# Kernel tuning notes

Measured on AMD Instinct MI355X. Metric: run time of the kernel, lower is better.

The kernel has to match this reference:

```python
import jax, jax.numpy as jnp
import numpy as np

NUM_NODES = 200000
EMB_DIM = 64
NUM_EDGES = 6400000
NUM_LAYERS = 4


def setup_inputs() -> dict:
    key = jax.random.key(0)
    k1, k2, k3, k4 = jax.random.split(key, 4)
    embeds = jax.random.normal(k1, (NUM_NODES, EMB_DIM), dtype=jnp.float32)
    adj_rows = jax.random.randint(k2, (NUM_EDGES,), 0, NUM_NODES, dtype=jnp.int64)
    adj_cols = jax.random.randint(k3, (NUM_EDGES,), 0, NUM_NODES, dtype=jnp.int64)
    adj_vals = jax.random.uniform(k4, (NUM_EDGES,), dtype=jnp.float32)
    return {"embeds": embeds, "adj_rows": adj_rows, "adj_cols": adj_cols, "adj_vals": adj_vals}


def _spmm(rows, cols, vals, x):
    # Sparse (COO) adjacency @ dense x: out[r] += v * x[c]
    msgs = vals[:, None] * x[cols]  # [E, d] gather + scale
    return jax.ops.segment_sum(msgs, rows, num_segments=NUM_NODES)


def reference(embeds, adj_rows, adj_cols, adj_vals):
    x = embeds
    acc = x  # running sum over layer outputs (fuses stack+mean)
    for _ in range(NUM_LAYERS):
        x = _spmm(adj_rows, adj_cols, adj_vals, x)
        acc = acc + x
    return acc / jnp.float32(NUM_LAYERS + 1)
```

## Files before the change

kernel.cpp:

```cpp
#include <hip/hip_runtime.h>

#define N_NODES 200000
#define DIM 64
#define BSHIFT 8
#define BROWS 256
#define NB 782
#define NB_PAD 1024
#define CHUNK 4096

__device__ __forceinline__ float bf2f(unsigned short u) {
    return __uint_as_float(((unsigned int)u) << 16);
}
__device__ __forceinline__ unsigned short f2bf(float f) {
    unsigned int u = __float_as_uint(f);
    u += 0x7FFFu + ((u >> 16) & 1u);
    return (unsigned short)(u >> 16);
}

__global__ __launch_bounds__(256) void bucket_hist(const int* __restrict__ rows, int E,
                                                   int* __restrict__ bcnt) {
    __shared__ int h[NB_PAD];
    for (int i = threadIdx.x; i < NB_PAD; i += 256) h[i] = 0;
    __syncthreads();
    int stride = gridDim.x * blockDim.x;
    for (int e = blockIdx.x * blockDim.x + threadIdx.x; e < E; e += stride)
        atomicAdd(&h[rows[e] >> BSHIFT], 1);
    __syncthreads();
    for (int i = threadIdx.x; i < NB; i += 256)
        if (h[i]) atomicAdd(&bcnt[i], h[i]);
}

__global__ __launch_bounds__(1024) void bucket_scan(const int* __restrict__ bcnt,
                                                    int* __restrict__ bbase,
                                                    int* __restrict__ bcur) {
    __shared__ int wsum[16];
    int t = threadIdx.x;
    int v = (t < NB) ? bcnt[t] : 0;
    int incl = v;
    for (int off = 1; off < 64; off <<= 1) {
        int u = __shfl_up(incl, off);
        if ((t & 63) >= off) incl += u;
    }
    if ((t & 63) == 63) wsum[t >> 6] = incl;
    __syncthreads();
    if (t < 16) {
        int w = wsum[t];
        for (int off = 1; off < 16; off <<= 1) {
            int u = __shfl_up(w, off);
            if (t >= off) w += u;
        }
        wsum[t] = w;
    }
    __syncthreads();
    int wb = (t >= 64) ? wsum[(t >> 6) - 1] : 0;
    int excl = wb + incl - v;
    if (t < NB) { bbase[t] = excl; bcur[t] = excl; }
    if (t == NB - 1) bbase[NB] = excl + v;
}

__global__ __launch_bounds__(512) void bucket_scatter(const int* __restrict__ rows,
                                                      const int* __restrict__ cols,
                                                      const float* __restrict__ vals, int E,
                                                      int* __restrict__ bcur,
                                                      int2* __restrict__ tmp) {
    __shared__ int h[NB_PAD];
    __shared__ int cur2[NB_PAD];
    __shared__ int wtot[8];
    __shared__ int2 stage[CHUNK];
    __shared__ unsigned short sbkt[CHUNK];
    const int base = blockIdx.x * CHUNK;
    const int count = min(CHUNK, E - base);
    const int t = threadIdx.x;

    for (int i = t; i < NB_PAD; i += 512) h[i] = 0;
    __syncthreads();

    int myr[8], myc[8];
    float myv[8];
#pragma unroll
    for (int k = 0; k < 8; ++k) {
        int i = t + k * 512;
        if (i < count) {
            myr[k] = rows[base + i];
            myc[k] = cols[base + i];
            myv[k] = vals[base + i];
            atomicAdd(&h[myr[k] >> BSHIFT], 1);
        }
    }
    __syncthreads();

    int h0 = h[2 * t], h1 = h[2 * t + 1];
    int s = h0 + h1;
    int incl = s;
    for (int off = 1; off < 64; off <<= 1) {
        int u = __shfl_up(incl, off);
        if ((t & 63) >= off) incl += u;
    }
    if ((t & 63) == 63) wtot[t >> 6] = incl;
    __syncthreads();
    int wb = 0;
    for (int w = 0; w < (t >> 6); ++w) wb += wtot[w];
    int excl = wb + incl - s;
    cur2[2 * t] = excl;
    cur2[2 * t + 1] = excl + h0;
    __syncthreads();

    for (int i = t; i < NB; i += 512) {
        int hi = h[i];
        int g = hi ? atomicAdd(&bcur[i], hi) : 0;
        h[i] = g - cur2[i];
    }
    __syncthreads();

#pragma unroll
    for (int k = 0; k < 8; ++k) {
        int i = t + k * 512;
        if (i < count) {
            int r = myr[k];
            int b = r >> BSHIFT;
            int slot = atomicAdd(&cur2[b], 1);
            stage[slot] = make_int2(((r & (BROWS - 1)) << 18) | myc[k], __float_as_int(myv[k]));
            sbkt[slot] = (unsigned short)b;
        }
    }
    __syncthreads();
    for (int s2 = t; s2 < count; s2 += 512)
        tmp[s2 + h[sbkt[s2]]] = stage[s2];
}

__global__ __launch_bounds__(512) void bucket_sort(const int2* __restrict__ tmp,
                                                   const int* __restrict__ bbase,
                                                   int2* __restrict__ sorted,
                                                   int* __restrict__ row_start) {
    __shared__ int h[BROWS];
    __shared__ int hbase[BROWS];
    __shared__ int wtot[4];
    const int b = blockIdx.x;
    const int s0 = bbase[b], s1 = bbase[b + 1];
    const int t = threadIdx.x;
    if (t < BROWS) h[t] = 0;
    __syncthreads();
    for (int e = s0 + t; e < s1; e += 512)
        atomicAdd(&h[tmp[e].x >> 18], 1);
    __syncthreads();
    int v = 0, incl = 0;
    if (t < BROWS) {
        v = h[t];
        incl = v;
        for (int off = 1; off < 64; off <<= 1) {
            int u = __shfl_up(incl, off);
            if ((t & 63) >= off) incl += u;
        }
        if ((t & 63) == 63) wtot[t >> 6] = incl;
    }
    __syncthreads();
    if (t < BROWS) {
        int wb = 0;
        for (int w = 0; w < (t >> 6); ++w) wb += wtot[w];
        hbase[t] = wb + incl - v;
    }
    __syncthreads();
    if (t < BROWS) {
        h[t] = hbase[t];
        int row = (b << BSHIFT) + t;
        if (row < N_NODES) row_start[row] = s0 + hbase[t];
    }
    if (b == NB - 1 && t == 0) row_start[N_NODES] = s1;
    __syncthreads();
    for (int e = s0 + t; e < s1; e += 512) {
        int2 kv = tmp[e];
        int r = kv.x >> 18;
        int rank = atomicAdd(&h[r], 1);
        sorted[s0 + rank] = make_int2(kv.x & 0x3FFFF, kv.y);
    }
}

__global__ __launch_bounds__(256) void convert_kernel(const float* __restrict__ src,
                                                      unsigned short* __restrict__ dst, int n4) {
    int i = blockIdx.x * blockDim.x + threadIdx.x;
    if (i >= n4) return;
    float4 v = *(const float4*)(src + i * 4);
    ushort4 o;
    o.x = f2bf(v.x); o.y = f2bf(v.y); o.z = f2bf(v.z); o.w = f2bf(v.w);
    *(ushort4*)(dst + i * 4) = o;
}

#define BF_LO(u) __uint_as_float((u) << 16)
#define BF_HI(u) __uint_as_float((u) & 0xFFFF0000u)
#define FMA8(G, V)                              \
    do {                                        \
        a0 = fmaf((V), BF_LO((G).x), a0);       \
        a1 = fmaf((V), BF_HI((G).x), a1);       \
        a2 = fmaf((V), BF_LO((G).y), a2);       \
        a3 = fmaf((V), BF_HI((G).y), a3);       \
        a4 = fmaf((V), BF_LO((G).z), a4);       \
        a5 = fmaf((V), BF_HI((G).z), a5);       \
        a6 = fmaf((V), BF_LO((G).w), a6);       \
        a7 = fmaf((V), BF_HI((G).w), a7);       \
    } while (0)

template <int MODE>
__global__ __launch_bounds__(256) void spmm_kernel(const int2* __restrict__ sorted,
                                                   const int* __restrict__ row_start,
                                                   const unsigned short* __restrict__ xb,
                                                   const float* __restrict__ embeds,
                                                   unsigned short* __restrict__ y,
                                                   float* __restrict__ acc) {
    int gid = blockIdx.x * blockDim.x + threadIdx.x;
    int r = gid >> 3;
    if (r >= N_NODES) return;
    int j = (gid & 7) << 3;
    const unsigned short* xbj = xb + j;
    int e = row_start[r], eend = row_start[r + 1];
    float a0 = 0.f, a1 = 0.f, a2 = 0.f, a3 = 0.f, a4 = 0.f, a5 = 0.f, a6 = 0.f, a7 = 0.f;

    int2 c0 = make_int2(0, 0), c1 = make_int2(0, 0);
    int2 c2 = make_int2(0, 0), c3 = make_int2(0, 0);
    if (e + 4 <= eend) {
        c0 = sorted[e]; c1 = sorted[e + 1]; c2 = sorted[e + 2]; c3 = sorted[e + 3];
    }
    while (e + 8 <= eend) {
        uint4 g0 = *(const uint4*)(xbj + (c0.x << 6));
        uint4 g1 = *(const uint4*)(xbj + (c1.x << 6));
        uint4 g2 = *(const uint4*)(xbj + (c2.x << 6));
        uint4 g3 = *(const uint4*)(xbj + (c3.x << 6));
        int2 n0 = sorted[e + 4], n1 = sorted[e + 5];
        int2 n2 = sorted[e + 6], n3 = sorted[e + 7];
        float v0 = __int_as_float(c0.y), v1 = __int_as_float(c1.y);
        float v2 = __int_as_float(c2.y), v3 = __int_as_float(c3.y);
        FMA8(g0, v0); FMA8(g1, v1); FMA8(g2, v2); FMA8(g3, v3);
        c0 = n0; c1 = n1; c2 = n2; c3 = n3;
        e += 4;
    }
    if (e + 4 <= eend) {
        uint4 g0 = *(const uint4*)(xbj + (c0.x << 6));
        uint4 g1 = *(const uint4*)(xbj + (c1.x << 6));
        uint4 g2 = *(const uint4*)(xbj + (c2.x << 6));
        uint4 g3 = *(const uint4*)(xbj + (c3.x << 6));
        float v0 = __int_as_float(c0.y), v1 = __int_as_float(c1.y);
        float v2 = __int_as_float(c2.y), v3 = __int_as_float(c3.y);
        FMA8(g0, v0); FMA8(g1, v1); FMA8(g2, v2); FMA8(g3, v3);
        e += 4;
    }
    for (; e < eend; ++e) {
        int2 cv = sorted[e];
        uint4 g = *(const uint4*)(xbj + (cv.x << 6));
        float v = __int_as_float(cv.y);
        FMA8(g, v);
    }

    int o = (r << 6) + j;
    if (MODE == 0) {
        uint4 yo;
        yo.x = (unsigned)f2bf(a0) | ((unsigned)f2bf(a1) << 16);
        yo.y = (unsigned)f2bf(a2) | ((unsigned)f2bf(a3) << 16);
        yo.z = (unsigned)f2bf(a4) | ((unsigned)f2bf(a5) << 16);
        yo.w = (unsigned)f2bf(a6) | ((unsigned)f2bf(a7) << 16);
        *(uint4*)(y + o) = yo;
        float4 x0 = *(const float4*)(embeds + o);
        float4 x1 = *(const float4*)(embeds + o + 4);
        *(float4*)(acc + o)     = make_float4(x0.x + a0, x0.y + a1, x0.z + a2, x0.w + a3);
        *(float4*)(acc + o + 4) = make_float4(x1.x + a4, x1.y + a5, x1.z + a6, x1.w + a7);
    } else if (MODE == 1) {
        uint4 yo;
        yo.x = (unsigned)f2bf(a0) | ((unsigned)f2bf(a1) << 16);
        yo.y = (unsigned)f2bf(a2) | ((unsigned)f2bf(a3) << 16);
        yo.z = (unsigned)f2bf(a4) | ((unsigned)f2bf(a5) << 16);
        yo.w = (unsigned)f2bf(a6) | ((unsigned)f2bf(a7) << 16);
        *(uint4*)(y + o) = yo;
        float4 q0 = *(const float4*)(acc + o);
        float4 q1 = *(const float4*)(acc + o + 4);
        *(float4*)(acc + o)     = make_float4(q0.x + a0, q0.y + a1, q0.z + a2, q0.w + a3);
        *(float4*)(acc + o + 4) = make_float4(q1.x + a4, q1.y + a5, q1.z + a6, q1.w + a7);
    } else {
        const float sc = 0.2f;
        float4 q0 = *(const float4*)(acc + o);
        float4 q1 = *(const float4*)(acc + o + 4);
        *(float4*)(acc + o)     = make_float4((q0.x + a0) * sc, (q0.y + a1) * sc,
                                              (q0.z + a2) * sc, (q0.w + a3) * sc);
        *(float4*)(acc + o + 4) = make_float4((q1.x + a4) * sc, (q1.y + a5) * sc,
                                              (q1.z + a6) * sc, (q1.w + a7) * sc);
    }
}

extern "C" void kernel_launch(void* const* d_in, const int* in_sizes, int n_in,
                              void* d_out, int out_size, void* d_ws, size_t ws_size,
                              hipStream_t stream) {
    const float* embeds = (const float*)d_in[0];
    const int*   rows   = (const int*)d_in[1];
    const int*   cols   = (const int*)d_in[2];
    const float* vals   = (const float*)d_in[3];
    float* acc = (float*)d_out;
    const int E = in_sizes[1];

    char* ws = (char*)d_ws;
    size_t off = 0;
    auto alloc = [&](size_t bytes) -> char* {
        char* p = ws + off;
        off = (off + bytes + 255) & ~(size_t)255;
        return p;
    };
    int*   bcnt      = (int*)alloc((size_t)NB * 4);
    int*   bbase     = (int*)alloc((size_t)(NB + 1) * 4);
    int*   bcur      = (int*)alloc((size_t)NB * 4);
    int*   row_start = (int*)alloc((size_t)(N_NODES + 1) * 4);
    int2*  sorted    = (int2*)alloc((size_t)E * 8);
    unsigned short* xb0 = (unsigned short*)alloc((size_t)N_NODES * DIM * 2);
    unsigned short* xb1 = (unsigned short*)alloc((size_t)N_NODES * DIM * 2);
    int2*  tmp       = (int2*)alloc((size_t)E * 8);

    hipMemsetAsync(bcnt, 0, (size_t)NB * 4, stream);

    bucket_hist<<<1024, 256, 0, stream>>>(rows, E, bcnt);
    bucket_scan<<<1, 1024, 0, stream>>>(bcnt, bbase, bcur);
    bucket_scatter<<<(E + CHUNK - 1) / CHUNK, 512, 0, stream>>>(rows, cols, vals, E, bcur, tmp);
    bucket_sort<<<NB, 512, 0, stream>>>(tmp, bbase, sorted, row_start);

    int n4 = N_NODES * DIM / 4;
    convert_kernel<<<(n4 + 255) / 256, 256, 0, stream>>>(embeds, xb0, n4);

    int sb = (N_NODES * 8 + 255) / 256;
    spmm_kernel<0><<<sb, 256, 0, stream>>>(sorted, row_start, xb0, embeds, xb1, acc);
    spmm_kernel<1><<<sb, 256, 0, stream>>>(sorted, row_start, xb1, embeds, xb0, acc);
    spmm_kernel<1><<<sb, 256, 0, stream>>>(sorted, row_start, xb0, embeds, xb1, acc);
    spmm_kernel<2><<<sb, 256, 0, stream>>>(sorted, row_start, xb1, embeds, xb0, acc);
}
```

Measured before the change: 823.2 us.

## Partition edges into column stripes for per-row CSR segments per stripe

Edges are now bucketed by column stripe (8 stripes of 25000 nodes) and then by destination-row block, producing eight CSR row_start arrays, one per stripe. In SpMM each row walks stripe 0 through 7 in turn, so threads running at similar times gather from the same 25000-node slice of x and that slice can stay resident in cache. The costs are a bigger sort (3128 buckets, more bucket_sort blocks, a smaller scatter chunk), eight row_start reads per row, and the loss of the old software prefetch of the next edge group. Because stripes are processed in order within each row, rows run concurrently are not kept on the same stripe, so the gain in cache locality is uncertain.

Result: slower. 895.3 us (+8.8%).

```diff
diff --git a/kernel.cpp b/kernel.cpp
--- a/kernel.cpp
+++ b/kernel.cpp
@@ -2,31 +2,36 @@
 
 #define N_NODES 200000
 #define DIM 64
-#define BSHIFT 8
-#define BROWS 256
-#define NB 782
-#define NB_PAD 1024
-#define CHUNK 4096
-
-__device__ __forceinline__ float bf2f(unsigned short u) {
-    return __uint_as_float(((unsigned int)u) << 16);
-}
+#define NS 8
+#define SROWS 25000
+#define DSHIFT 9
+#define DROWS 512
+#define NDB 391
+#define NB2 (NS * NDB)
+#define NB2_PAD 4096
+#define CHUNK 2048
+#define RSP (N_NODES + 1)
+
 __device__ __forceinline__ unsigned short f2bf(float f) {
     unsigned int u = __float_as_uint(f);
     u += 0x7FFFu + ((u >> 16) & 1u);
     return (unsigned short)(u >> 16);
 }
-
-__global__ __launch_bounds__(256) void bucket_hist(const int* __restrict__ rows, int E,
+__device__ __forceinline__ int stripe_of(int c) { return (int)((unsigned)c / 25000u); }
+
+__global__ __launch_bounds__(256) void bucket_hist(const int* __restrict__ rows,
+                                                   const int* __restrict__ cols, int E,
                                                    int* __restrict__ bcnt) {
-    __shared__ int h[NB_PAD];
-    for (int i = threadIdx.x; i < NB_PAD; i += 256) h[i] = 0;
+    __shared__ int h[NB2];
+    for (int i = threadIdx.x; i < NB2; i += 256) h[i] = 0;
     __syncthreads();
     int stride = gridDim.x * blockDim.x;
-    for (int e = blockIdx.x * blockDim.x + threadIdx.x; e < E; e += stride)
-        atomicAdd(&h[rows[e] >> BSHIFT], 1);
-    __syncthreads();
-    for (int i = threadIdx.x; i < NB; i += 256)
+    for (int e = blockIdx.x * blockDim.x + threadIdx.x; e < E; e += stride) {
+        int cb = stripe_of(cols[e]) * NDB + (rows[e] >> DSHIFT);
+        atomicAdd(&h[cb], 1);
+    }
+    __syncthreads();
+    for (int i = threadIdx.x; i < NB2; i += 256)
         if (h[i]) atomicAdd(&bcnt[i], h[i]);
 }
 
@@ -35,8 +40,13 @@
                                                     int* __restrict__ bcur) {
     __shared__ int wsum[16];
     int t = threadIdx.x;
-    int v = (t < NB) ? bcnt[t] : 0;
-    int incl = v;
+    int idx = 4 * t;
+    int v0 = (idx + 0 < NB2) ? bcnt[idx + 0] : 0;
+    int v1 = (idx + 1 < NB2) ? bcnt[idx + 1] : 0;
+    int v2 = (idx + 2 < NB2) ? bcnt[idx + 2] : 0;
+    int v3 = (idx + 3 < NB2) ? bcnt[idx + 3] : 0;
+    int ssum = v0 + v1 + v2 + v3;
+    int incl = ssum;
     for (int off = 1; off < 64; off <<= 1) {
         int u = __shfl_up(incl, off);
         if ((t & 63) >= off) incl += u;
@@ -53,9 +63,14 @@
     }
     __syncthreads();
     int wb = (t >= 64) ? wsum[(t >> 6) - 1] : 0;
-    int excl = wb + incl - v;
-    if (t < NB) { bbase[t] = excl; bcur[t] = excl; }
-    if (t == NB - 1) bbase[NB] = excl + v;
+    int run = wb + incl - ssum;
+    if (idx + 0 < NB2) { bbase[idx + 0] = run; bcur[idx + 0] = run; } else if (idx + 0 == NB2) bbase[NB2] = run;
+    run += v0;
+    if (idx + 1 < NB2) { bbase[idx + 1] = run; bcur[idx + 1] = run; } else if (idx + 1 == NB2) bbase[NB2] = run;
+    run += v1;
+    if (idx + 2 < NB2) { bbase[idx + 2] = run; bcur[idx + 2] = run; } else if (idx + 2 == NB2) bbase[NB2] = run;
+    run += v2;
+    if (idx + 3 < NB2) { bbase[idx + 3] = run; bcur[idx + 3] = run; } else if (idx + 3 == NB2) bbase[NB2] = run;
 }
 
 __global__ __launch_bounds__(512) void bucket_scatter(const int* __restrict__ rows,
@@ -63,8 +78,8 @@
                                                       const float* __restrict__ vals, int E,
                                                       int* __restrict__ bcur,
                                                       int2* __restrict__ tmp) {
-    __shared__ int h[NB_PAD];
-    __shared__ int cur2[NB_PAD];
+    __shared__ int h[NB2_PAD];
+    __shared__ int cur2[NB2_PAD];
     __shared__ int wtot[8];
     __shared__ int2 stage[CHUNK];
     __shared__ unsigned short sbkt[CHUNK];
@@ -72,26 +87,28 @@
     const int count = min(CHUNK, E - base);
     const int t = threadIdx.x;
 
-    for (int i = t; i < NB_PAD; i += 512) h[i] = 0;
-    __syncthreads();
-
-    int myr[8], myc[8];
-    float myv[8];
-#pragma unroll
-    for (int k = 0; k < 8; ++k) {
+    for (int i = t; i < NB2_PAD; i += 512) h[i] = 0;
+    __syncthreads();
+
+    int myr[4], myc[4], myb[4];
+    float myv[4];
+#pragma unroll
+    for (int k = 0; k < 4; ++k) {
         int i = t + k * 512;
         if (i < count) {
             myr[k] = rows[base + i];
             myc[k] = cols[base + i];
             myv[k] = vals[base + i];
-            atomicAdd(&h[myr[k] >> BSHIFT], 1);
-        }
-    }
-    __syncthreads();
-
-    int h0 = h[2 * t], h1 = h[2 * t + 1];
-    int s = h0 + h1;
-    int incl = s;
+            myb[k] = stripe_of(myc[k]) * NDB + (myr[k] >> DSHIFT);
+            atomicAdd(&h[myb[k]], 1);
+        }
+    }
+    __syncthreads();
+
+    int b[8], ssum = 0;
+#pragma unroll
+    for (int k = 0; k < 8; ++k) { b[k] = h[8 * t + k]; ssum += b[k]; }
+    int incl = ssum;
     for (int off = 1; off < 64; off <<= 1) {
         int u = __shfl_up(incl, off);
         if ((t & 63) >= off) incl += u;
@@ -100,12 +117,12 @@
     __syncthreads();
     int wb = 0;
     for (int w = 0; w < (t >> 6); ++w) wb += wtot[w];
-    int excl = wb + incl - s;
-    cur2[2 * t] = excl;
-    cur2[2 * t + 1] = excl + h0;
-    __syncthreads();
-
-    for (int i = t; i < NB; i += 512) {
+    int run = wb + incl - ssum;
+#pragma unroll
+    for (int k = 0; k < 8; ++k) { cur2[8 * t + k] = run; run += b[k]; }
+    __syncthreads();
+
+    for (int i = t; i < NB2; i += 512) {
         int hi = h[i];
         int g = hi ? atomicAdd(&bcur[i], hi) : 0;
         h[i] = g - cur2[i];
@@ -113,14 +130,13 @@
     __syncthreads();
 
 #pragma unroll
-    for (int k = 0; k < 8; ++k) {
+    for (int k = 0; k < 4; ++k) {
         int i = t + k * 512;
         if (i < count) {
-            int r = myr[k];
-            int b = r >> BSHIFT;
-            int slot = atomicAdd(&cur2[b], 1);
-            stage[slot] = make_int2(((r & (BROWS - 1)) << 18) | myc[k], __float_as_int(myv[k]));
-            sbkt[slot] = (unsigned short)b;
+            int slot = atomicAdd(&cur2[myb[k]], 1);
+            stage[slot] = make_int2(((myr[k] & (DROWS - 1)) << 18) | myc[k],
+                                    __float_as_int(myv[k]));
+            sbkt[slot] = (unsigned short)myb[k];
         }
     }
     __syncthreads();
@@ -132,40 +148,35 @@
                                                    const int* __restrict__ bbase,
                                                    int2* __restrict__ sorted,
                                                    int* __restrict__ row_start) {
-    __shared__ int h[BROWS];
-    __shared__ int hbase[BROWS];
-    __shared__ int wtot[4];
-    const int b = blockIdx.x;
-    const int s0 = bbase[b], s1 = bbase[b + 1];
+    __shared__ int h[DROWS];
+    __shared__ int hbase[DROWS];
+    __shared__ int wtot[8];
+    const int bk = blockIdx.x;
+    const int s0 = bbase[bk], s1 = bbase[bk + 1];
     const int t = threadIdx.x;
-    if (t < BROWS) h[t] = 0;
+    h[t] = 0;
     __syncthreads();
     for (int e = s0 + t; e < s1; e += 512)
         atomicAdd(&h[tmp[e].x >> 18], 1);
     __syncthreads();
-    int v = 0, incl = 0;
-    if (t < BROWS) {
-        v = h[t];
-        incl = v;
-        for (int off = 1; off < 64; off <<= 1) {
-            int u = __shfl_up(incl, off);
-            if ((t & 63) >= off) incl += u;
-        }
-        if ((t & 63) == 63) wtot[t >> 6] = incl;
-    }
-    __syncthreads();
-    if (t < BROWS) {
-        int wb = 0;
-        for (int w = 0; w < (t >> 6); ++w) wb += wtot[w];
-        hbase[t] = wb + incl - v;
-    }
-    __syncthreads();
-    if (t < BROWS) {
-        h[t] = hbase[t];
-        int row = (b << BSHIFT) + t;
-        if (row < N_NODES) row_start[row] = s0 + hbase[t];
-    }
-    if (b == NB - 1 && t == 0) row_start[N_NODES] = s1;
+    int v = h[t];
+    int incl = v;
+    for (int off = 1; off < 64; off <<= 1) {
+        int u = __shfl_up(incl, off);
+        if ((t & 63) >= off) incl += u;
+    }
+    if ((t & 63) == 63) wtot[t >> 6] = incl;
+    __syncthreads();
+    int wb = 0;
+    for (int w = 0; w < (t >> 6); ++w) wb += wtot[w];
+    hbase[t] = wb + incl - v;
+    __syncthreads();
+    h[t] = hbase[t];
+    int stripe = bk / NDB;
+    int db = bk - stripe * NDB;
+    int row = (db << DSHIFT) + t;
+    if (row < N_NODES) row_start[stripe * RSP + row] = s0 + hbase[t];
+    if (db == NDB - 1 && t == 0) row_start[stripe * RSP + N_NODES] = s1;
     __syncthreads();
     for (int e = s0 + t; e < s1; e += 512) {
         int2 kv = tmp[e];
@@ -211,42 +222,32 @@
     if (r >= N_NODES) return;
     int j = (gid & 7) << 3;
     const unsigned short* xbj = xb + j;
-    int e = row_start[r], eend = row_start[r + 1];
     float a0 = 0.f, a1 = 0.f, a2 = 0.f, a3 = 0.f, a4 = 0.f, a5 = 0.f, a6 = 0.f, a7 = 0.f;
 
-    int2 c0 = make_int2(0, 0), c1 = make_int2(0, 0);
-    int2 c2 = make_int2(0, 0), c3 = make_int2(0, 0);
-    if (e + 4 <= eend) {
-        c0 = sorted[e]; c1 = sorted[e + 1]; c2 = sorted[e + 2]; c3 = sorted[e + 3];
-    }
-    while (e + 8 <= eend) {
-        uint4 g0 = *(const uint4*)(xbj + (c0.x << 6));
-        uint4 g1 = *(const uint4*)(xbj + (c1.x << 6));
-        uint4 g2 = *(const uint4*)(xbj + (c2.x << 6));
-        uint4 g3 = *(const uint4*)(xbj + (c3.x << 6));
-        int2 n0 = sorted[e + 4], n1 = sorted[e + 5];
-        int2 n2 = sorted[e + 6], n3 = sorted[e + 7];
-        float v0 = __int_as_float(c0.y), v1 = __int_as_float(c1.y);
-        float v2 = __int_as_float(c2.y), v3 = __int_as_float(c3.y);
-        FMA8(g0, v0); FMA8(g1, v1); FMA8(g2, v2); FMA8(g3, v3);
-        c0 = n0; c1 = n1; c2 = n2; c3 = n3;
-        e += 4;
-    }
-    if (e + 4 <= eend) {
-        uint4 g0 = *(const uint4*)(xbj + (c0.x << 6));
-        uint4 g1 = *(const uint4*)(xbj + (c1.x << 6));
-        uint4 g2 = *(const uint4*)(xbj + (c2.x << 6));
-        uint4 g3 = *(const uint4*)(xbj + (c3.x << 6));
-        float v0 = __int_as_float(c0.y), v1 = __int_as_float(c1.y);
-        float v2 = __int_as_float(c2.y), v3 = __int_as_float(c3.y);
-        FMA8(g0, v0); FMA8(g1, v1); FMA8(g2, v2); FMA8(g3, v3);
-        e += 4;
-    }
-    for (; e < eend; ++e) {
-        int2 cv = sorted[e];
-        uint4 g = *(const uint4*)(xbj + (cv.x << 6));
-        float v = __int_as_float(cv.y);
-        FMA8(g, v);
+#pragma unroll
+    for (int s = 0; s < NS; ++s) {
+        const int* rs = row_start + s * RSP + r;
+        int e = rs[0], eend = rs[1];
+        while (e + 4 <= eend) {
+            int2 c0 = sorted[e];
+            int2 c1 = sorted[e + 1];
+            int2 c2 = sorted[e + 2];
+            int2 c3 = sorted[e + 3];
+            uint4 g0 = *(const uint4*)(xbj + (c0.x << 6));
+            uint4 g1 = *(const uint4*)(xbj + (c1.x << 6));
+            uint4 g2 = *(const uint4*)(xbj + (c2.x << 6));
+            uint4 g3 = *(const uint4*)(xbj + (c3.x << 6));
+            float v0 = __int_as_float(c0.y), v1 = __int_as_float(c1.y);
+            float v2 = __int_as_float(c2.y), v3 = __int_as_float(c3.y);
+            FMA8(g0, v0); FMA8(g1, v1); FMA8(g2, v2); FMA8(g3, v3);
+            e += 4;
+        }
+        for (; e < eend; ++e) {
+            int2 cv = sorted[e];
+            uint4 g = *(const uint4*)(xbj + (cv.x << 6));
+            float v = __int_as_float(cv.y);
+            FMA8(g, v);
+        }
     }
 
     int o = (r << 6) + j;
@@ -300,21 +301,21 @@
         off = (off + bytes + 255) & ~(size_t)255;
         return p;
     };
-    int*   bcnt      = (int*)alloc((size_t)NB * 4);
-    int*   bbase     = (int*)alloc((size_t)(NB + 1) * 4);
-    int*   bcur      = (int*)alloc((size_t)NB * 4);
-    int*   row_start = (int*)alloc((size_t)(N_NODES + 1) * 4);
+    int*   bcnt      = (int*)alloc((size_t)NB2 * 4);
+    int*   bbase     = (int*)alloc((size_t)(NB2 + 1) * 4);
+    int*   bcur      = (int*)alloc((size_t)NB2 * 4);
+    int*   row_start = (int*)alloc((size_t)NS * RSP * 4);
     int2*  sorted    = (int2*)alloc((size_t)E * 8);
     unsigned short* xb0 = (unsigned short*)alloc((size_t)N_NODES * DIM * 2);
     unsigned short* xb1 = (unsigned short*)alloc((size_t)N_NODES * DIM * 2);
     int2*  tmp       = (int2*)alloc((size_t)E * 8);
 
-    hipMemsetAsync(bcnt, 0, (size_t)NB * 4, stream);
-
-    bucket_hist<<<1024, 256, 0, stream>>>(rows, E, bcnt);
+    hipMemsetAsync(bcnt, 0, (size_t)NB2 * 4, stream);
+
+    bucket_hist<<<1024, 256, 0, stream>>>(rows, cols, E, bcnt);
     bucket_scan<<<1, 1024, 0, stream>>>(bcnt, bbase, bcur);
     bucket_scatter<<<(E + CHUNK - 1) / CHUNK, 512, 0, stream>>>(rows, cols, vals, E, bcur, tmp);
-    bucket_sort<<<NB, 512, 0, stream>>>(tmp, bbase, sorted, row_start);
+    bucket_sort<<<NB2, 512, 0, stream>>>(tmp, bbase, sorted, row_start);
 
     int n4 = N_NODES * DIM / 4;
     convert_kernel<<<(n4 + 255) / 256, 256, 0, stream>>>(embeds, xb0, n4);
```
